# Kernel tuning notes

Hardware: AMD Instinct MI355X
Metric: run time of the kernel (lower is better)

Reference implementation:

```python
import jax, jax.numpy as jnp
import numpy as np

VOCAB = 50257
D = 256
N_UTT = 64
L = 512


def gru_scan(x, W_ih, W_hh, b_ih, b_hh):
    # torch nn.GRU (single layer, batch_first) semantics.
    # x: [B, T, d] -> outputs [B, T, d]
    B, T, d = x.shape
    gx = jnp.einsum('btd,gd->btg', x, W_ih) + b_ih  # [B, T, 3d] input gates precomputed
    gx = jnp.transpose(gx, (1, 0, 2))               # [T, B, 3d] for scan over time

    def step(h, gxt):
        gh = h @ W_hh.T + b_hh                      # [B, 3d]
        xr, xz, xn = jnp.split(gxt, 3, axis=-1)
        hr, hz, hn = jnp.split(gh, 3, axis=-1)
        r = jax.nn.sigmoid(xr + hr)
        z = jax.nn.sigmoid(xz + hz)
        n = jnp.tanh(xn + r * hn)
        h_new = (1.0 - z) * n + z * h
        return h_new, h_new

    h0 = jnp.zeros((B, d), x.dtype)
    _, hs = jax.lax.scan(step, h0, gx)              # hs: [T, B, d]
    return jnp.transpose(hs, (1, 0, 2))


def attn_pool(out, w, b):
    # out: [B, T, d]; Linear(d,1) -> softmax over T -> weighted sum
    logits = out @ w + b                            # [B, T]
    weights = jax.nn.softmax(logits, axis=-1)
    return jnp.einsum('bt,btd->bd', weights, out)   # [B, d]


def setup_inputs() -> dict:
    key = jax.random.key(0)
    ks = jax.random.split(key, 16)
    s = 1.0 / np.sqrt(D)
    u = lambda k, shape: jax.random.uniform(k, shape, jnp.float32, -s, s)
    return {
        'tokens': jax.random.randint(ks[0], (N_UTT, L), 0, VOCAB, dtype=jnp.int32),
        'embed': jax.random.normal(ks[1], (VOCAB, D), jnp.float32),
        'wg_Wih': u(ks[2], (3 * D, D)),
        'wg_Whh': u(ks[3], (3 * D, D)),
        'wg_bih': u(ks[4], (3 * D,)),
        'wg_bhh': u(ks[5], (3 * D,)),
        'ua_w': u(ks[6], (D,)),
        'ua_b': u(ks[7], ()),
        'sg_Wih': u(ks[8], (3 * D, D)),
        'sg_Whh': u(ks[9], (3 * D, D)),
        'sg_bih': u(ks[10], (3 * D,)),
        'sg_bhh': u(ks[11], (3 * D,)),
        'da_w': u(ks[12], (D,)),
        'da_b': u(ks[13], ()),
    }


def reference(tokens, embed, wg_Wih, wg_Whh, wg_bih, wg_bhh, ua_w, ua_b,
              sg_Wih, sg_Whh, sg_bih, sg_bhh, da_w, da_b):
    # Word level: embed each utterance, GRU, attention pooling (batched over utterances)
    emb = embed[tokens]                                   # [N, L, d]
    word_out = gru_scan(emb, wg_Wih, wg_Whh, wg_bih, wg_bhh)
    utt_vecs = attn_pool(word_out, ua_w, ua_b)            # [N, d]
    # Sentence level: pad_sequence of [1,d] vectors -> [N, 1, d] (batch=N, seq=1)
    sent_in = utt_vecs[:, None, :]                        # [N, 1, d]
    sent_out = gru_scan(sent_in, sg_Wih, sg_Whh, sg_bih, sg_bhh)
    dialog_vec = attn_pool(sent_out, da_w, da_b)          # [N, d] (softmax over seq len 1)
    return dialog_vec
```

## Files before the change

kernel.cpp:

```cpp
#include <hip/hip_runtime.h>

typedef _Float16 f16x8 __attribute__((ext_vector_type(8)));
typedef float f32x4 __attribute__((ext_vector_type(4)));

constexpr int D = 256;
constexpr int NUTT = 64;
constexpr int L = 512;
constexpr int G = 768;

__device__ __forceinline__ void lds_barrier() {
  asm volatile("s_waitcnt lgkmcnt(0)\n\ts_barrier" ::: "memory");
}

__device__ __forceinline__ float fast_rcp(float x) {
  return __builtin_amdgcn_rcpf(x);
}
__device__ __forceinline__ float sigm(float x) {
  return fast_rcp(1.0f + __expf(-x));
}
__device__ __forceinline__ float tanh_f(float x) {
  float ax = fabsf(x);
  float e = __expf(-2.0f * ax);
  float r = (1.0f - e) * fast_rcp(1.0f + e);
  return copysignf(r, x);
}

__global__ __launch_bounds__(256) void gx_gemm(
    const int* __restrict__ tokens, const float* __restrict__ embed,
    const float* __restrict__ Wih, const float* __restrict__ bih,
    float* __restrict__ gx) {
  __shared__ float As[64][33];
  __shared__ float Bs[32][129];
  __shared__ int toks[64];

  const int tid = threadIdx.x;
  const int m0 = blockIdx.x * 64;
  const int n0 = blockIdx.y * 128;
  if (tid < 64) toks[tid] = tokens[m0 + tid];
  __syncthreads();

  const int ty = tid >> 4;
  const int tx = tid & 15;
  float acc[4][8] = {};

  for (int k0 = 0; k0 < 256; k0 += 32) {
    {
      const int i = tid >> 2;
      const int kq = (tid & 3) * 4;
      const float* src = embed + (size_t)toks[i] * D + k0;
      float4 v0 = *(const float4*)(src + kq);
      float4 v1 = *(const float4*)(src + kq + 16);
      As[i][kq + 0] = v0.x; As[i][kq + 1] = v0.y;
      As[i][kq + 2] = v0.z; As[i][kq + 3] = v0.w;
      As[i][kq + 16] = v1.x; As[i][kq + 17] = v1.y;
      As[i][kq + 18] = v1.z; As[i][kq + 19] = v1.w;
    }
    {
      const int goff = tid >> 3;
      const int kq = (tid & 7) * 4;
      for (int gp = 0; gp < 128; gp += 32) {
        const float* src = Wih + (size_t)(n0 + goff + gp) * D + k0 + kq;
        float4 v = *(const float4*)src;
        Bs[kq + 0][goff + gp] = v.x;
        Bs[kq + 1][goff + gp] = v.y;
        Bs[kq + 2][goff + gp] = v.z;
        Bs[kq + 3][goff + gp] = v.w;
      }
    }
    __syncthreads();
    const int r0 = ty * 4;
#pragma unroll 4
    for (int k = 0; k < 32; ++k) {
      float a0 = As[r0 + 0][k], a1 = As[r0 + 1][k];
      float a2 = As[r0 + 2][k], a3 = As[r0 + 3][k];
#pragma unroll
      for (int cc = 0; cc < 8; ++cc) {
        float bv = Bs[k][tx + 16 * cc];
        acc[0][cc] = fmaf(a0, bv, acc[0][cc]);
        acc[1][cc] = fmaf(a1, bv, acc[1][cc]);
        acc[2][cc] = fmaf(a2, bv, acc[2][cc]);
        acc[3][cc] = fmaf(a3, bv, acc[3][cc]);
      }
    }
    __syncthreads();
  }
#pragma unroll
  for (int rr = 0; rr < 4; ++rr) {
    float* dst = gx + (size_t)(m0 + ty * 4 + rr) * G + n0;
#pragma unroll
    for (int cc = 0; cc < 8; ++cc) {
      int c = tx + 16 * cc;
      dst[c] = acc[rr][cc] + bih[n0 + c];
    }
  }
}

__global__ __launch_bounds__(512, 2) void gru_scan_word(
    const float* __restrict__ gx,
    const float* __restrict__ Whh,
    const float* __restrict__ bhh,
    float* __restrict__ wo) {
  __shared__ __align__(16) _Float16 hbuf[2][D];
  __shared__ __align__(16) float pre4[D][4];

  const int t = threadIdx.x;
  const int b = blockIdx.x;
  const int w = t >> 6;
  const int lane = t & 63;
  const int l15 = lane & 15;
  const int lk = lane >> 4;

  f16x8 Bf[6][8];
#pragma unroll
  for (int i = 0; i < 6; ++i) {
    const float* row = Whh + (size_t)(96 * w + 16 * i + l15) * D + 8 * lk;
#pragma unroll
    for (int f = 0; f < 8; ++f) {
      float4 v0 = *(const float4*)(row + 32 * f);
      float4 v1 = *(const float4*)(row + 32 * f + 4);
      Bf[i][f] = f16x8{(_Float16)v0.x, (_Float16)v0.y,
                       (_Float16)v0.z, (_Float16)v0.w,
                       (_Float16)v1.x, (_Float16)v1.y,
                       (_Float16)v1.z, (_Float16)v1.w};
    }
  }

  float bR = 0.0f, bZ = 0.0f, bN = 0.0f;
  float gr = 0.0f, gz = 0.0f, gn = 0.0f;
  const float* gxb = gx + (size_t)b * L * G;
  if (t < 256) {
    bR = bhh[t]; bZ = bhh[D + t]; bN = bhh[2 * D + t];
    gr = gxb[t]; gz = gxb[D + t]; gn = gxb[2 * D + t];
    hbuf[0][t] = (_Float16)0.0f;
  }
  float hprev = 0.0f;
  float* wob = wo + (size_t)b * L * D;
  __syncthreads();

  for (int ts = 0; ts < L; ++ts) {
    const int cur = ts & 1;

    const _Float16* hb = hbuf[cur];
    f16x8 A[8];
#pragma unroll
    for (int f = 0; f < 8; ++f)
      A[f] = *(const f16x8*)(hb + 32 * f + 8 * lk);

#pragma unroll
    for (int i = 0; i < 6; ++i) {
      f32x4 acc = {0.0f, 0.0f, 0.0f, 0.0f};
#pragma unroll
      for (int f = 0; f < 8; ++f)
        acc = __builtin_amdgcn_mfma_f32_16x16x32_f16(A[f], Bf[i][f], acc,
                                                     0, 0, 0);
      if (lk == 0) {
        const int n = 96 * w + 16 * i + l15;
        pre4[n & 255][n >> 8] = acc[0];
      }
    }
    lds_barrier();

    if (t < 256) {
      float4 pa = *(const float4*)pre4[t];
      float r = sigm(gr + pa.x + bR);
      float z = sigm(gz + pa.y + bZ);
      float nn = tanh_f(gn + r * (pa.z + bN));
      float hn = fmaf(z, hprev - nn, nn);
      hprev = hn;
      hbuf[cur ^ 1][t] = (_Float16)hn;
      wob[(size_t)ts * D + t] = hn;
      const int tn = (ts + 1 < L) ? ts + 1 : ts;
      const float* gxn = gxb + (size_t)tn * G;
      gr = gxn[t]; gz = gxn[D + t]; gn = gxn[2 * D + t];
    }
    lds_barrier();
  }
}

__global__ __launch_bounds__(256) void attn_pool_word(
    const float* __restrict__ wo, const float* __restrict__ uaw,
    float* __restrict__ utt) {
  __shared__ float wsh[D];
  __shared__ float lg[L];
  __shared__ float red[8];
  const int tid = threadIdx.x, b = blockIdx.x;
  wsh[tid] = uaw[tid];
  __syncthreads();

  const int wid = tid >> 6, lane = tid & 63;
  const float* base = wo + (size_t)b * L * D;
  for (int t = wid; t < L; t += 4) {
    const float* row = base + (size_t)t * D;
    float p = 0.0f;
#pragma unroll
    for (int j = 0; j < 4; ++j) p = fmaf(row[lane + 64 * j], wsh[lane + 64 * j], p);
#pragma unroll
    for (int off = 32; off; off >>= 1) p += __shfl_down(p, off);
    if (lane == 0) lg[t] = p;
  }
  __syncthreads();

  float m = fmaxf(lg[tid], lg[tid + 256]);
#pragma unroll
  for (int off = 32; off; off >>= 1) m = fmaxf(m, __shfl_down(m, off));
  if (lane == 0) red[wid] = m;
  __syncthreads();
  m = fmaxf(fmaxf(red[0], red[1]), fmaxf(red[2], red[3]));

  float e0 = __expf(lg[tid] - m), e1 = __expf(lg[tid + 256] - m);
  float s = e0 + e1;
#pragma unroll
  for (int off = 32; off; off >>= 1) s += __shfl_down(s, off);
  if (lane == 0) red[4 + wid] = s;
  __syncthreads();
  s = red[4] + red[5] + red[6] + red[7];
  float inv = 1.0f / s;
  lg[tid] = e0 * inv;
  lg[tid + 256] = e1 * inv;
  __syncthreads();

  float acc = 0.0f;
#pragma unroll 4
  for (int t = 0; t < L; ++t) acc = fmaf(lg[t], base[(size_t)t * D + tid], acc);
  utt[(size_t)b * D + tid] = acc;
}

__global__ __launch_bounds__(256) void sent_kernel(
    const float* __restrict__ utt, const float* __restrict__ Wih,
    const float* __restrict__ bih, const float* __restrict__ bhh,
    float* __restrict__ out) {
  __shared__ float u[D];
  const int d = threadIdx.x, b = blockIdx.x;
  u[d] = utt[(size_t)b * D + d];
  __syncthreads();

  const float* wr = Wih + (size_t)d * D;
  const float* wz = Wih + (size_t)(D + d) * D;
  const float* wn = Wih + (size_t)(2 * D + d) * D;
  float ar = 0.0f, az = 0.0f, an = 0.0f;
  for (int k = 0; k < D; k += 4) {
    float4 vr = *(const float4*)(wr + k);
    float4 vz = *(const float4*)(wz + k);
    float4 vn = *(const float4*)(wn + k);
    float u0 = u[k], u1 = u[k + 1], u2 = u[k + 2], u3 = u[k + 3];
    ar += vr.x * u0 + vr.y * u1 + vr.z * u2 + vr.w * u3;
    az += vz.x * u0 + vz.y * u1 + vz.z * u2 + vz.w * u3;
    an += vn.x * u0 + vn.y * u1 + vn.z * u2 + vn.w * u3;
  }
  float xr = ar + bih[d];
  float xz = az + bih[D + d];
  float xn = an + bih[2 * D + d];
  float r = sigm(xr + bhh[d]);
  float z = sigm(xz + bhh[D + d]);
  float n = tanh_f(xn + r * bhh[2 * D + d]);
  out[(size_t)b * D + d] = (1.0f - z) * n;
}

extern "C" void kernel_launch(void* const* d_in, const int* in_sizes, int n_in,
                              void* d_out, int out_size, void* d_ws, size_t ws_size,
                              hipStream_t stream) {
  const int* tokens    = (const int*)d_in[0];
  const float* embed   = (const float*)d_in[1];
  const float* wg_Wih  = (const float*)d_in[2];
  const float* wg_Whh  = (const float*)d_in[3];
  const float* wg_bih  = (const float*)d_in[4];
  const float* wg_bhh  = (const float*)d_in[5];
  const float* ua_w    = (const float*)d_in[6];
  const float* sg_Wih  = (const float*)d_in[8];
  const float* sg_bih  = (const float*)d_in[10];
  const float* sg_bhh  = (const float*)d_in[11];
  float* out = (float*)d_out;

  char* ws = (char*)d_ws;
  float* gx  = (float*)ws;
  float* wo  = (float*)(ws + (size_t)NUTT * L * G * 4);
  float* utt = (float*)(ws + (size_t)NUTT * L * G * 4
                           + (size_t)NUTT * L * D * 4);

  dim3 gB(512, 6);
  gx_gemm<<<gB, 256, 0, stream>>>(tokens, embed, wg_Wih, wg_bih, gx);
  gru_scan_word<<<NUTT, 512, 0, stream>>>(gx, wg_Whh, wg_bhh, wo);
  attn_pool_word<<<NUTT, 256, 0, stream>>>(wo, ua_w, utt);
  sent_kernel<<<NUTT, 256, 0, stream>>>(utt, sg_Wih, sg_bih, sg_bhh, out);
}
```

Before: 941.7 us.

## Split recurrent GEMV between MFMA and VALU dot2 paths per step

Each wave now computes half of its 96 recurrent-gate outputs with MFMA (3 tiles instead of 6) and the other half with packed fp16 dot2 instructions on the vector ALU, using weights held in registers and cross-lane shuffles for the reductions. The three MFMA chains are interleaved so they can issue back to back. The intent is to shorten the serial per-timestep latency by overlapping matrix-core and VALU work and by cutting the wasted MFMA work (only row 0 of each tile is used). This costs many more VGPRs for the register-held weights, which may cause spills or lower occupancy, and adds shuffle latency.

```diff
diff --git a/kernel.cpp b/kernel.cpp
--- a/kernel.cpp
+++ b/kernel.cpp
@@ -1,6 +1,7 @@
 #include <hip/hip_runtime.h>
 
 typedef _Float16 f16x8 __attribute__((ext_vector_type(8)));
+typedef _Float16 f16x2 __attribute__((ext_vector_type(2)));
 typedef float f32x4 __attribute__((ext_vector_type(4)));
 
 constexpr int D = 256;
@@ -10,6 +11,18 @@
 
 __device__ __forceinline__ void lds_barrier() {
   asm volatile("s_waitcnt lgkmcnt(0)\n\ts_barrier" ::: "memory");
+}
+
+__device__ __forceinline__ float fdot2(f16x2 a, f16x2 b, float c) {
+#if defined(__has_builtin)
+#if __has_builtin(__builtin_amdgcn_fdot2)
+  return __builtin_amdgcn_fdot2(a, b, c, false);
+#else
+  return c + (float)a.x * (float)b.x + (float)a.y * (float)b.y;
+#endif
+#else
+  return c + (float)a.x * (float)b.x + (float)a.y * (float)b.y;
+#endif
 }
 
 __device__ __forceinline__ float fast_rcp(float x) {
@@ -110,9 +123,9 @@
   const int l15 = lane & 15;
   const int lk = lane >> 4;
 
-  f16x8 Bf[6][8];
-#pragma unroll
-  for (int i = 0; i < 6; ++i) {
+  f16x8 Bf[3][8];
+#pragma unroll
+  for (int i = 0; i < 3; ++i) {
     const float* row = Whh + (size_t)(96 * w + 16 * i + l15) * D + 8 * lk;
 #pragma unroll
     for (int f = 0; f < 8; ++f) {
@@ -125,6 +138,29 @@
     }
   }
 
+  const int khA = lane >> 5;
+  const int kqB = lane >> 4;
+  f16x2 wA[64];
+  {
+    const float* row = Whh + (size_t)(96 * w + 48 + (lane & 31)) * D + khA * 128;
+#pragma unroll
+    for (int c = 0; c < 32; ++c) {
+      float4 v = *(const float4*)(row + 4 * c);
+      wA[2 * c]     = f16x2{(_Float16)v.x, (_Float16)v.y};
+      wA[2 * c + 1] = f16x2{(_Float16)v.z, (_Float16)v.w};
+    }
+  }
+  f16x2 wB[32];
+  {
+    const float* row = Whh + (size_t)(96 * w + 80 + l15) * D + kqB * 64;
+#pragma unroll
+    for (int c = 0; c < 16; ++c) {
+      float4 v = *(const float4*)(row + 4 * c);
+      wB[2 * c]     = f16x2{(_Float16)v.x, (_Float16)v.y};
+      wB[2 * c + 1] = f16x2{(_Float16)v.z, (_Float16)v.w};
+    }
+  }
+
   float bR = 0.0f, bZ = 0.0f, bN = 0.0f;
   float gr = 0.0f, gz = 0.0f, gn = 0.0f;
   const float* gxb = gx + (size_t)b * L * G;
@@ -139,24 +175,66 @@
 
   for (int ts = 0; ts < L; ++ts) {
     const int cur = ts & 1;
-
     const _Float16* hb = hbuf[cur];
+
     f16x8 A[8];
 #pragma unroll
     for (int f = 0; f < 8; ++f)
       A[f] = *(const f16x8*)(hb + 32 * f + 8 * lk);
 
-#pragma unroll
-    for (int i = 0; i < 6; ++i) {
-      f32x4 acc = {0.0f, 0.0f, 0.0f, 0.0f};
-#pragma unroll
-      for (int f = 0; f < 8; ++f)
-        acc = __builtin_amdgcn_mfma_f32_16x16x32_f16(A[f], Bf[i][f], acc,
-                                                     0, 0, 0);
-      if (lk == 0) {
-        const int n = 96 * w + 16 * i + l15;
-        pre4[n & 255][n >> 8] = acc[0];
-      }
+    f32x4 acc0 = {0.f, 0.f, 0.f, 0.f};
+    f32x4 acc1 = {0.f, 0.f, 0.f, 0.f};
+    f32x4 acc2 = {0.f, 0.f, 0.f, 0.f};
+#pragma unroll
+    for (int f = 0; f < 8; ++f) {
+      acc0 = __builtin_amdgcn_mfma_f32_16x16x32_f16(A[f], Bf[0][f], acc0, 0, 0, 0);
+      acc1 = __builtin_amdgcn_mfma_f32_16x16x32_f16(A[f], Bf[1][f], acc1, 0, 0, 0);
+      acc2 = __builtin_amdgcn_mfma_f32_16x16x32_f16(A[f], Bf[2][f], acc2, 0, 0, 0);
+    }
+
+    const f16x8* hA8 = (const f16x8*)(hb + khA * 128);
+    const f16x8* hB8 = (const f16x8*)(hb + kqB * 64);
+    float pA0 = 0.0f, pA1 = 0.0f, pB0 = 0.0f, pB1 = 0.0f;
+#pragma unroll
+    for (int c = 0; c < 16; ++c) {
+      union { f16x8 v; f16x2 h[4]; } U;
+      U.v = hA8[c];
+      pA0 = fdot2(wA[4 * c + 0], U.h[0], pA0);
+      pA1 = fdot2(wA[4 * c + 1], U.h[1], pA1);
+      pA0 = fdot2(wA[4 * c + 2], U.h[2], pA0);
+      pA1 = fdot2(wA[4 * c + 3], U.h[3], pA1);
+    }
+#pragma unroll
+    for (int c = 0; c < 8; ++c) {
+      union { f16x8 v; f16x2 h[4]; } U;
+      U.v = hB8[c];
+      pB0 = fdot2(wB[4 * c + 0], U.h[0], pB0);
+      pB1 = fdot2(wB[4 * c + 1], U.h[1], pB1);
+      pB0 = fdot2(wB[4 * c + 2], U.h[2], pB0);
+      pB1 = fdot2(wB[4 * c + 3], U.h[3], pB1);
+    }
+
+    float pA = pA0 + pA1;
+    pA += __shfl_xor(pA, 32);
+    float pB = pB0 + pB1;
+    pB += __shfl_xor(pB, 16);
+    pB += __shfl_xor(pB, 32);
+
+    if (lane < 32) {
+      const int n = 96 * w + 48 + lane;
+      pre4[n & 255][n >> 8] = pA;
+    }
+    if (lane < 16) {
+      const int n = 96 * w + 80 + lane;
+      pre4[n & 255][n >> 8] = pB;
+    }
+    if (lk == 0) {
+      const int n0t = 96 * w + l15;
+      pre4[n0t & 255][n0t >> 8] = acc0[0];
+      const int n1t = 96 * w + 16 + l15;
+      pre4[n1t & 255][n1t >> 8] = acc1[0];
+      const int n2t = 96 * w + 32 + l15;
+      pre4[n2t & 255][n2t >> 8] = acc2[0];
     }
     lds_barrier();
 
```

Measured after the change: 1.387 ms. 1.47x slower.

## Compute input-gate GEMM with split-fp16 MFMA instead of scalar FMA

Applied to the files above, without the earlier changes.

Replaces the LDS-tiled fp32 scalar-FMA input projection GEMM with an MFMA kernel. Each fp32 operand is split into fp16 hi and lo parts, and three MFMAs (hi*hi, lo*hi, hi*lo) per step recover near-fp32 accuracy. A small pre-kernel splits W_ih into hi/lo halves stored in the word-output workspace region, which is reused before the scan writes it. The scan kernel's LDS staging is also changed from an interleaved [D][4] layout to a [3][D] layout. The cost is an extra launch and dropping the lo*lo term, which adds a small precision risk.

```diff
diff --git a/kernel.cpp b/kernel.cpp
--- a/kernel.cpp
+++ b/kernel.cpp
@@ -25,72 +25,67 @@
   return copysignf(r, x);
 }
 
-__global__ __launch_bounds__(256) void gx_gemm(
+__global__ __launch_bounds__(256) void split_wih(
+    const float* __restrict__ Wih, _Float16* __restrict__ hi,
+    _Float16* __restrict__ lo) {
+  const int i = blockIdx.x * 256 + threadIdx.x;
+  float v = Wih[i];
+  _Float16 h = (_Float16)v;
+  hi[i] = h;
+  lo[i] = (_Float16)(v - (float)h);
+}
+
+__global__ __launch_bounds__(256) void gx_gemm_mfma(
     const int* __restrict__ tokens, const float* __restrict__ embed,
-    const float* __restrict__ Wih, const float* __restrict__ bih,
-    float* __restrict__ gx) {
-  __shared__ float As[64][33];
-  __shared__ float Bs[32][129];
-  __shared__ int toks[64];
-
+    const _Float16* __restrict__ whi, const _Float16* __restrict__ wlo,
+    const float* __restrict__ bih, float* __restrict__ gx) {
   const int tid = threadIdx.x;
   const int m0 = blockIdx.x * 64;
   const int n0 = blockIdx.y * 128;
-  if (tid < 64) toks[tid] = tokens[m0 + tid];
-  __syncthreads();
-
-  const int ty = tid >> 4;
-  const int tx = tid & 15;
-  float acc[4][8] = {};
-
-  for (int k0 = 0; k0 < 256; k0 += 32) {
-    {
-      const int i = tid >> 2;
-      const int kq = (tid & 3) * 4;
-      const float* src = embed + (size_t)toks[i] * D + k0;
-      float4 v0 = *(const float4*)(src + kq);
-      float4 v1 = *(const float4*)(src + kq + 16);
-      As[i][kq + 0] = v0.x; As[i][kq + 1] = v0.y;
-      As[i][kq + 2] = v0.z; As[i][kq + 3] = v0.w;
-      As[i][kq + 16] = v1.x; As[i][kq + 17] = v1.y;
-      As[i][kq + 18] = v1.z; As[i][kq + 19] = v1.w;
-    }
-    {
-      const int goff = tid >> 3;
-      const int kq = (tid & 7) * 4;
-      for (int gp = 0; gp < 128; gp += 32) {
-        const float* src = Wih + (size_t)(n0 + goff + gp) * D + k0 + kq;
-        float4 v = *(const float4*)src;
-        Bs[kq + 0][goff + gp] = v.x;
-        Bs[kq + 1][goff + gp] = v.y;
-        Bs[kq + 2][goff + gp] = v.z;
-        Bs[kq + 3][goff + gp] = v.w;
-      }
-    }
-    __syncthreads();
-    const int r0 = ty * 4;
-#pragma unroll 4
-    for (int k = 0; k < 32; ++k) {
-      float a0 = As[r0 + 0][k], a1 = As[r0 + 1][k];
-      float a2 = As[r0 + 2][k], a3 = As[r0 + 3][k];
-#pragma unroll
-      for (int cc = 0; cc < 8; ++cc) {
-        float bv = Bs[k][tx + 16 * cc];
-        acc[0][cc] = fmaf(a0, bv, acc[0][cc]);
-        acc[1][cc] = fmaf(a1, bv, acc[1][cc]);
-        acc[2][cc] = fmaf(a2, bv, acc[2][cc]);
-        acc[3][cc] = fmaf(a3, bv, acc[3][cc]);
-      }
-    }
-    __syncthreads();
-  }
-#pragma unroll
-  for (int rr = 0; rr < 4; ++rr) {
-    float* dst = gx + (size_t)(m0 + ty * 4 + rr) * G + n0;
-#pragma unroll
-    for (int cc = 0; cc < 8; ++cc) {
-      int c = tx + 16 * cc;
-      dst[c] = acc[rr][cc] + bih[n0 + c];
+
+  const int w = tid >> 6;
+  const int lane = tid & 63;
+  const int l15 = lane & 15;
+  const int lk = lane >> 4;
+
+  const int tok = tokens[m0 + 16 * w + l15];
+  const float* arow = embed + (size_t)tok * D;
+
+  f32x4 acc[8] = {};
+  const _Float16* bh0 = whi + (size_t)(n0 + l15) * D + 8 * lk;
+  const _Float16* bl0 = wlo + (size_t)(n0 + l15) * D + 8 * lk;
+
+#pragma unroll
+  for (int f = 0; f < 8; ++f) {
+    const float* ap = arow + 32 * f + 8 * lk;
+    float4 v0 = *(const float4*)(ap);
+    float4 v1 = *(const float4*)(ap + 4);
+    float av[8] = {v0.x, v0.y, v0.z, v0.w, v1.x, v1.y, v1.z, v1.w};
+    f16x8 ahi, alo;
+#pragma unroll
+    for (int j = 0; j < 8; ++j) {
+      _Float16 h = (_Float16)av[j];
+      ahi[j] = h;
+      alo[j] = (_Float16)(av[j] - (float)h);
+    }
+#pragma unroll
+    for (int i = 0; i < 8; ++i) {
+      f16x8 bhi = *(const f16x8*)(bh0 + (size_t)(16 * i) * D + 32 * f);
+      f16x8 blo = *(const f16x8*)(bl0 + (size_t)(16 * i) * D + 32 * f);
+      acc[i] = __builtin_amdgcn_mfma_f32_16x16x32_f16(ahi, bhi, acc[i], 0, 0, 0);
+      acc[i] = __builtin_amdgcn_mfma_f32_16x16x32_f16(alo, bhi, acc[i], 0, 0, 0);
+      acc[i] = __builtin_amdgcn_mfma_f32_16x16x32_f16(ahi, blo, acc[i], 0, 0, 0);
+    }
+  }
+
+#pragma unroll
+  for (int i = 0; i < 8; ++i) {
+    const int n = n0 + 16 * i + l15;
+    const float bb = bih[n];
+#pragma unroll
+    for (int reg = 0; reg < 4; ++reg) {
+      const int m = m0 + 16 * w + 4 * lk + reg;
+      gx[(size_t)m * G + n] = acc[i][reg] + bb;
     }
   }
 }
@@ -101,7 +96,7 @@
     const float* __restrict__ bhh,
     float* __restrict__ wo) {
   __shared__ __align__(16) _Float16 hbuf[2][D];
-  __shared__ __align__(16) float pre4[D][4];
+  __shared__ float pre[3][D];
 
   const int t = threadIdx.x;
   const int b = blockIdx.x;
@@ -155,16 +150,16 @@
                                                      0, 0, 0);
       if (lk == 0) {
         const int n = 96 * w + 16 * i + l15;
-        pre4[n & 255][n >> 8] = acc[0];
+        pre[n >> 8][n & 255] = acc[0];
       }
     }
     lds_barrier();
 
     if (t < 256) {
-      float4 pa = *(const float4*)pre4[t];
-      float r = sigm(gr + pa.x + bR);
-      float z = sigm(gz + pa.y + bZ);
-      float nn = tanh_f(gn + r * (pa.z + bN));
+      float aR = pre[0][t], aZ = pre[1][t], aN = pre[2][t];
+      float r = sigm(gr + aR + bR);
+      float z = sigm(gz + aZ + bZ);
+      float nn = tanh_f(gn + r * (aN + bN));
       float hn = fmaf(z, hprev - nn, nn);
       hprev = hn;
       hbuf[cur ^ 1][t] = (_Float16)hn;
@@ -273,12 +268,16 @@
 
   char* ws = (char*)d_ws;
   float* gx  = (float*)ws;
-  float* wo  = (float*)(ws + (size_t)NUTT * L * G * 4);
-  float* utt = (float*)(ws + (size_t)NUTT * L * G * 4
-                           + (size_t)NUTT * L * D * 4);
-
+  char* wo_region = ws + (size_t)NUTT * L * G * 4;
+  float* wo  = (float*)wo_region;
+  float* utt = (float*)(wo_region + (size_t)NUTT * L * D * 4);
+
+  _Float16* whi = (_Float16*)wo_region;
+  _Float16* wlo = whi + (size_t)G * D;
+
+  split_wih<<<G, 256, 0, stream>>>(wg_Wih, whi, wlo);
   dim3 gB(512, 6);
-  gx_gemm<<<gB, 256, 0, stream>>>(tokens, embed, wg_Wih, wg_bih, gx);
+  gx_gemm_mfma<<<gB, 256, 0, stream>>>(tokens, embed, whi, wlo, wg_bih, gx);
   gru_scan_word<<<NUTT, 512, 0, stream>>>(gx, wg_Whh, wg_bhh, wo);
   attn_pool_word<<<NUTT, 256, 0, stream>>>(wo, ua_w, utt);
   sent_kernel<<<NUTT, 256, 0, stream>>>(utt, sg_Wih, sg_bih, sg_bhh, out);
```

After: 970.8 us. 3.1% more time.
